# Optimization experiments

Hardware: AMD Instinct MI355X
Metric: run time of the kernel (lower is better)

The kernel has to match this reference:

```python
import jax, jax.numpy as jnp
import numpy as np

N_NODES = 4096        # number of sum nodes in this layer
N_CHILD = 16384       # total number of child-layer nodes
DEGREE = 64           # fan-in per sum node
NNZ = N_NODES * DEGREE
BATCH = 128


def setup_inputs() -> dict:
    key = jax.random.key(0)
    k1, k2, k3 = jax.random.split(key, 3)
    child_ll = jax.random.normal(k1, (BATCH, N_CHILD), dtype=jnp.float32)
    log_w = jax.random.normal(k2, (NNZ,), dtype=jnp.float32)
    # each sum node has exactly DEGREE incoming edges (sorted segment ids)
    rows = jnp.repeat(jnp.arange(N_NODES, dtype=jnp.int32), DEGREE)
    cols = jax.random.randint(k3, (NNZ,), 0, N_CHILD, dtype=jnp.int32)
    return {"child_ll": child_ll, "log_w": log_w, "rows": rows, "cols": cols}


def _segment_logsumexp(v, seg, num_segments):
    # v: [E, ...], seg: [E] -> [num_segments, ...], numerically stable
    m = jax.ops.segment_max(v, seg, num_segments=num_segments)
    m = jax.lax.stop_gradient(m)
    s = jax.ops.segment_sum(jnp.exp(v - m[seg]), seg, num_segments=num_segments)
    return m + jnp.log(s)


def reference(child_ll, log_w, rows, cols):
    # per-edge weighted child log-likelihood: [E, B]
    v = child_ll.T[cols] + log_w[:, None]
    # unnormalized sum-node log-likelihood: [N, B]
    ll = _segment_logsumexp(v, rows, N_NODES)
    # per-node log normalization constant logsumexp(log_w) over each row: [N]
    log_z = _segment_logsumexp(log_w, rows, N_NODES)
    return (ll - log_z[:, None]).T  # [B, N]
```

## Files before the change

### kernel.cpp

```cpp
#include <hip/hip_runtime.h>

#define N_NODES 4096
#define N_CHILD 16384
#define DEGREE  64
#define BATCH   128

__global__ __launch_bounds__(256)
void transpose_kernel(const float* __restrict__ in, float* __restrict__ out) {
    __shared__ float tile[32][33];
    const int c0 = blockIdx.x * 32;
    const int b0 = blockIdx.y * 32;
    const int tx = threadIdx.x;
    const int ty = threadIdx.y;
#pragma unroll
    for (int j = 0; j < 32; j += 8) {
        tile[ty + j][tx] = in[(size_t)(b0 + ty + j) * N_CHILD + (c0 + tx)];
    }
    __syncthreads();
#pragma unroll
    for (int j = 0; j < 32; j += 8) {
        out[(size_t)(c0 + ty + j) * BATCH + (b0 + tx)] = tile[tx][ty + j];
    }
}

__global__ __launch_bounds__(128)
void sum_layer_kernel(const float* __restrict__ childT,
                      const float* __restrict__ log_w,
                      const int*   __restrict__ cols,
                      float* __restrict__ out)
{
    const int n = blockIdx.x;
    const int b = threadIdx.x;

    __shared__ int   cols_s[DEGREE];
    __shared__ float w_s[DEGREE];
    __shared__ float lz_s;

    float w = 0.0f;
    if (b < DEGREE) {
        const int e = n * DEGREE + b;
        const int c = cols[e];
        w = log_w[e];
        cols_s[b] = c;
        w_s[b]    = w;
        float m = w;
#pragma unroll
        for (int off = 32; off >= 1; off >>= 1)
            m = fmaxf(m, __shfl_xor(m, off));
        float s = __expf(w - m);
#pragma unroll
        for (int off = 32; off >= 1; off >>= 1)
            s += __shfl_xor(s, off);
        if (b == 0) lz_s = m + __logf(s);
    }
    __syncthreads();

    const float* base = childT + b;
    float v[DEGREE];
#pragma unroll
    for (int d = 0; d < DEGREE; ++d) {
        v[d] = base[(size_t)cols_s[d] * BATCH] + w_s[d];
    }

    float m = v[0];
#pragma unroll
    for (int d = 1; d < DEGREE; ++d) m = fmaxf(m, v[d]);
    float s = 0.0f;
#pragma unroll
    for (int d = 0; d < DEGREE; ++d) s += __expf(v[d] - m);

    out[(size_t)b * N_NODES + n] = m + __logf(s) - lz_s;
}

extern "C" void kernel_launch(void* const* d_in, const int* in_sizes, int n_in,
                              void* d_out, int out_size, void* d_ws, size_t ws_size,
                              hipStream_t stream) {
    const float* child_ll = (const float*)d_in[0];
    const float* log_w    = (const float*)d_in[1];
    const int*   cols     = (const int*)d_in[3];
    float*       out      = (float*)d_out;
    float*       childT   = (float*)d_ws;

    dim3 tb(32, 8);
    dim3 tg(N_CHILD / 32, BATCH / 32);
    transpose_kernel<<<tg, tb, 0, stream>>>(child_ll, childT);

    sum_layer_kernel<<<N_NODES, 128, 0, stream>>>(childT, log_w, cols, out);
}
```

Baseline: 87.09 us.

## Use chunked online logsumexp, coalesced transposed output, and drop shared staging

Replaces the 64-element register array with an online logsumexp over chunks of 16 edges. This cuts register pressure and should raise occupancy. The strided per-batch output write becomes a coalesced write into a node-major scratch buffer, followed by a third transpose kernel into [B, N]. cols and log_w are now read directly from global memory (uniform per block) rather than staged in shared memory, at the cost of an extra kernel launch and an extra pass over the output.

```diff
diff --git a/kernel.cpp b/kernel.cpp
--- a/kernel.cpp
+++ b/kernel.cpp
@@ -4,45 +4,39 @@
 #define N_CHILD 16384
 #define DEGREE  64
 #define BATCH   128
+#define CH      16
 
 __global__ __launch_bounds__(256)
-void transpose_kernel(const float* __restrict__ in, float* __restrict__ out) {
+void transpose_kernel(const float* __restrict__ in, float* __restrict__ out,
+                      int R, int C) {
     __shared__ float tile[32][33];
     const int c0 = blockIdx.x * 32;
-    const int b0 = blockIdx.y * 32;
+    const int r0 = blockIdx.y * 32;
     const int tx = threadIdx.x;
     const int ty = threadIdx.y;
 #pragma unroll
-    for (int j = 0; j < 32; j += 8) {
-        tile[ty + j][tx] = in[(size_t)(b0 + ty + j) * N_CHILD + (c0 + tx)];
-    }
+    for (int j = 0; j < 32; j += 8)
+        tile[ty + j][tx] = in[(size_t)(r0 + ty + j) * C + (c0 + tx)];
     __syncthreads();
 #pragma unroll
-    for (int j = 0; j < 32; j += 8) {
-        out[(size_t)(c0 + ty + j) * BATCH + (b0 + tx)] = tile[tx][ty + j];
-    }
+    for (int j = 0; j < 32; j += 8)
+        out[(size_t)(c0 + ty + j) * R + (r0 + tx)] = tile[tx][ty + j];
 }
 
 __global__ __launch_bounds__(128)
 void sum_layer_kernel(const float* __restrict__ childT,
                       const float* __restrict__ log_w,
                       const int*   __restrict__ cols,
-                      float* __restrict__ out)
+                      float* __restrict__ outT)
 {
     const int n = blockIdx.x;
     const int b = threadIdx.x;
+    const int ebase = n * DEGREE;
 
-    __shared__ int   cols_s[DEGREE];
-    __shared__ float w_s[DEGREE];
     __shared__ float lz_s;
 
-    float w = 0.0f;
     if (b < DEGREE) {
-        const int e = n * DEGREE + b;
-        const int c = cols[e];
-        w = log_w[e];
-        cols_s[b] = c;
-        w_s[b]    = w;
+        float w = log_w[ebase + b];
         float m = w;
 #pragma unroll
         for (int off = 32; off >= 1; off >>= 1)
@@ -53,23 +47,44 @@
             s += __shfl_xor(s, off);
         if (b == 0) lz_s = m + __logf(s);
     }
-    __syncthreads();
 
-    const float* base = childT + b;
-    float v[DEGREE];
+    float m_run, s_run;
+    {
+        float v[CH];
 #pragma unroll
-    for (int d = 0; d < DEGREE; ++d) {
-        v[d] = base[(size_t)cols_s[d] * BATCH] + w_s[d];
+        for (int j = 0; j < CH; ++j) {
+            const int e = ebase + j;
+            v[j] = childT[(size_t)cols[e] * BATCH + b] + log_w[e];
+        }
+        float mc = v[0];
+#pragma unroll
+        for (int j = 1; j < CH; ++j) mc = fmaxf(mc, v[j]);
+        float sc = 0.0f;
+#pragma unroll
+        for (int j = 0; j < CH; ++j) sc += __expf(v[j] - mc);
+        m_run = mc; s_run = sc;
+    }
+#pragma unroll
+    for (int chunk = 1; chunk < DEGREE / CH; ++chunk) {
+        float v[CH];
+#pragma unroll
+        for (int j = 0; j < CH; ++j) {
+            const int e = ebase + chunk * CH + j;
+            v[j] = childT[(size_t)cols[e] * BATCH + b] + log_w[e];
+        }
+        float mc = v[0];
+#pragma unroll
+        for (int j = 1; j < CH; ++j) mc = fmaxf(mc, v[j]);
+        float sc = 0.0f;
+#pragma unroll
+        for (int j = 0; j < CH; ++j) sc += __expf(v[j] - mc);
+        const float mn = fmaxf(m_run, mc);
+        s_run = s_run * __expf(m_run - mn) + sc * __expf(mc - mn);
+        m_run = mn;
     }
 
-    float m = v[0];
-#pragma unroll
-    for (int d = 1; d < DEGREE; ++d) m = fmaxf(m, v[d]);
-    float s = 0.0f;
-#pragma unroll
-    for (int d = 0; d < DEGREE; ++d) s += __expf(v[d] - m);
-
-    out[(size_t)b * N_NODES + n] = m + __logf(s) - lz_s;
+    __syncthreads();
+    outT[(size_t)n * BATCH + b] = m_run + __logf(s_run) - lz_s;
 }
 
 extern "C" void kernel_launch(void* const* d_in, const int* in_sizes, int n_in,
@@ -79,11 +94,19 @@
     const float* log_w    = (const float*)d_in[1];
     const int*   cols     = (const int*)d_in[3];
     float*       out      = (float*)d_out;
-    float*       childT   = (float*)d_ws;
 
-    dim3 tb(32, 8);
-    dim3 tg(N_CHILD / 32, BATCH / 32);
-    transpose_kernel<<<tg, tb, 0, stream>>>(child_ll, childT);
+    float* childT = (float*)d_ws;
+    float* outT   = (float*)((char*)d_ws + (size_t)N_CHILD * BATCH * 4);
 
-    sum_layer_kernel<<<N_NODES, 128, 0, stream>>>(childT, log_w, cols, out);
+    {
+        dim3 tb(32, 8), tg(N_CHILD / 32, BATCH / 32);
+        transpose_kernel<<<tg, tb, 0, stream>>>(child_ll, childT, BATCH, N_CHILD);
+    }
+
+    sum_layer_kernel<<<N_NODES, 128, 0, stream>>>(childT, log_w, cols, outT);
+
+    {
+        dim3 tb(32, 8), tg(BATCH / 32, N_NODES / 32);
+        transpose_kernel<<<tg, tb, 0, stream>>>(outT, out, N_NODES, BATCH);
+    }
 }
```

Measured after the change: 83.08 us. -4.6%, faster.
